# Kernel optimization log

Measured on AMD Instinct MI355X. Metric: run time of the kernel, lower is better.

Reference implementation:

```python
import jax, jax.numpy as jnp
import numpy as np

D_MODEL, N_HEADS, D_FF = 1024, 16, 4096
D_HEAD = D_MODEL // N_HEADS
B, S = 2, 2048
EPS = 1e-5


def setup_inputs() -> dict:
    key = jax.random.key(0)
    ks = jax.random.split(key, 12)
    sd = 1.0 / np.sqrt(D_MODEL)
    return {
        "x": jax.random.normal(ks[0], (B, S, D_MODEL), jnp.float32),
        "relative_bias": jax.random.normal(ks[1], (1, N_HEADS, S, S), jnp.float32),
        # attention projections, stored as (in, out) so y = x @ W
        "wq": jax.random.normal(ks[2], (D_MODEL, D_MODEL), jnp.float32) * sd,
        "wk": jax.random.normal(ks[3], (D_MODEL, D_MODEL), jnp.float32) * sd,
        "wv": jax.random.normal(ks[4], (D_MODEL, D_MODEL), jnp.float32) * sd,
        "wo": jax.random.normal(ks[5], (D_MODEL, D_MODEL), jnp.float32) * sd,
        "wo_b": jnp.zeros((D_MODEL,), jnp.float32),
        # FFN
        "w1": jax.random.normal(ks[6], (D_MODEL, D_FF), jnp.float32) * sd,
        "b1": jnp.zeros((D_FF,), jnp.float32),
        "w2": jax.random.normal(ks[7], (D_FF, D_MODEL), jnp.float32) * (1.0 / np.sqrt(D_FF)),
        "b2": jnp.zeros((D_MODEL,), jnp.float32),
        # LayerNorms
        "ln1_g": jnp.ones((D_MODEL,), jnp.float32),
        "ln1_b": jnp.zeros((D_MODEL,), jnp.float32),
        "ln2_g": jnp.ones((D_MODEL,), jnp.float32),
        "ln2_b": jnp.zeros((D_MODEL,), jnp.float32),
    }


def _layernorm(x, g, b):
    mu = jnp.mean(x, axis=-1, keepdims=True)
    var = jnp.mean(jnp.square(x - mu), axis=-1, keepdims=True)
    return (x - mu) * jax.lax.rsqrt(var + EPS) * g + b


def _attn(x, relative_bias, wq, wk, wv, wo, wo_b):
    b, s, d = x.shape
    # (B,S,D) -> (B,H,S,Dh)
    def split_heads(t):
        return t.reshape(b, s, N_HEADS, D_HEAD).transpose(0, 2, 1, 3)
    q = split_heads(x @ wq)
    k = split_heads(x @ wk)
    v = split_heads(x @ wv)
    scores = jnp.einsum("bhqd,bhkd->bhqk", q, k) / np.sqrt(D_HEAD) + relative_bias
    attn = jax.nn.softmax(scores, axis=-1)
    ctx = jnp.einsum("bhqk,bhkd->bhqd", attn, v)
    ctx = ctx.transpose(0, 2, 1, 3).reshape(b, s, d)
    return ctx @ wo + wo_b


def _ffn(x, w1, b1, w2, b2):
    return jax.nn.gelu(x @ w1 + b1, approximate=False) @ w2 + b2


def reference(x, relative_bias, wq, wk, wv, wo, wo_b, w1, b1, w2, b2,
              ln1_g, ln1_b, ln2_g, ln2_b):
    x = x + _attn(_layernorm(x, ln1_g, ln1_b), relative_bias, wq, wk, wv, wo, wo_b)
    x = x + _ffn(_layernorm(x, ln2_g, ln2_b), w1, b1, w2, b2)
    return x
```

## Files before the change

kernel.cpp:

```cpp
#include <hip/hip_runtime.h>
#include <hip/hip_bf16.h>
#include <stdint.h>

typedef unsigned short u16;
typedef __bf16 bf16x8 __attribute__((ext_vector_type(8)));
typedef u16   u16x8  __attribute__((ext_vector_type(8)));
typedef u16   u16x4  __attribute__((ext_vector_type(4)));
typedef u16   u16x2  __attribute__((ext_vector_type(2)));
typedef float f32x4  __attribute__((ext_vector_type(4)));

__device__ __forceinline__ u16 f2bf(float f) {
  union { float f; uint32_t u; } v; v.f = f;
  uint32_t r = v.u + 0x7fffu + ((v.u >> 16) & 1u);
  return (u16)(r >> 16);
}

typedef __attribute__((address_space(1))) void gvoid_t;
typedef __attribute__((address_space(3))) void lvoid_t;
__device__ __forceinline__ void gload_lds16(const void* g, void* l) {
  __builtin_amdgcn_global_load_lds((gvoid_t*)g, (lvoid_t*)l, 16, 0, 0);
}

__device__ __forceinline__ void barrier_lgkm() {
  asm volatile("s_waitcnt lgkmcnt(0)\ns_barrier" ::: "memory");
}
__device__ __forceinline__ void bar_only() {
  asm volatile("s_barrier" ::: "memory");
}
template<int N> __device__ __forceinline__ void wait_vm() {
  asm volatile("s_waitcnt vmcnt(%0)" :: "n"(N) : "memory");
}

template<int CTRL>
__device__ __forceinline__ float dpp_f(float x) {
  int i = __builtin_bit_cast(int, x);
  i = __builtin_amdgcn_update_dpp(i, i, CTRL, 0xF, 0xF, true);
  return __builtin_bit_cast(float, i);
}
__device__ __forceinline__ float rowmax16(float x) {
  x = fmaxf(x, dpp_f<0x128>(x));
  x = fmaxf(x, dpp_f<0x124>(x));
  x = fmaxf(x, dpp_f<0x122>(x));
  x = fmaxf(x, dpp_f<0x121>(x));
  return x;
}
__device__ __forceinline__ float rowsum16(float x) {
  x += dpp_f<0x128>(x);
  x += dpp_f<0x124>(x);
  x += dpp_f<0x122>(x);
  x += dpp_f<0x121>(x);
  return x;
}

__global__ __launch_bounds__(256)
void ln_kernel(const float* __restrict__ x, const float* __restrict__ g,
               const float* __restrict__ b, u16* __restrict__ out) {
  const int row = blockIdx.x;
  const int tid = threadIdx.x;
  const float* xr = x + (size_t)row * 1024;
  f32x4 v = *(const f32x4*)&xr[tid * 4];
  float s = v[0] + v[1] + v[2] + v[3];
  float q = v[0]*v[0] + v[1]*v[1] + v[2]*v[2] + v[3]*v[3];
  #pragma unroll
  for (int o = 32; o > 0; o >>= 1) { s += __shfl_xor(s, o); q += __shfl_xor(q, o); }
  __shared__ float ss[4], qq[4];
  if ((tid & 63) == 0) { ss[tid >> 6] = s; qq[tid >> 6] = q; }
  __syncthreads();
  s = ss[0] + ss[1] + ss[2] + ss[3];
  q = qq[0] + qq[1] + qq[2] + qq[3];
  float mu = s * (1.0f / 1024.0f);
  float var = q * (1.0f / 1024.0f) - mu * mu;
  float rstd = rsqrtf(var + 1e-5f);
  u16x4 o4;
  #pragma unroll
  for (int i = 0; i < 4; ++i)
    o4[i] = f2bf((v[i] - mu) * rstd * g[tid * 4 + i] + b[tid * 4 + i]);
  *(u16x4*)&out[(size_t)row * 1024 + tid * 4] = o4;
}

__global__ __launch_bounds__(256)
void transpose_cast(const float* __restrict__ W, u16* __restrict__ Wt, int K, int N) {
  __shared__ float t[32][33];
  const int n0 = blockIdx.x * 32, k0 = blockIdx.y * 32;
  const int tx = threadIdx.x & 31, ty = threadIdx.x >> 5;
  #pragma unroll
  for (int i = 0; i < 4; ++i)
    t[ty + 8*i][tx] = W[(size_t)(k0 + ty + 8*i) * N + n0 + tx];
  __syncthreads();
  #pragma unroll
  for (int i = 0; i < 4; ++i)
    Wt[(size_t)(n0 + ty + 8*i) * K + k0 + tx] = f2bf(t[tx][ty + 8*i]);
}

template<int EPI>
__global__ __launch_bounds__(256, 2)
void gemm_bt(const u16* __restrict__ A, const u16* __restrict__ Bt,
             void* __restrict__ out, const float* __restrict__ bias,
             const float* __restrict__ resid, int M, int N, int K) {
  __shared__ u16 As[2][128 * 32];
  __shared__ u16 Bs[2][128 * 32];
  const int tid = threadIdx.x;
  const int w = tid >> 6, l = tid & 63;
  const int bm = blockIdx.x * 128, bn = blockIdx.y * 128;
  const int wr = (w >> 1) * 64, wc = (w & 1) * 64;
  const int l15 = l & 15, lhi = l >> 4;
  f32x4 acc[4][4] = {};

  const int r4 = tid >> 2;
  const int c8 = (tid & 3) * 8;
  const u16* ga0 = A  + (size_t)(bm + r4) * K + c8;
  const u16* ga1 = ga0 + (size_t)64 * K;
  const u16* gb0 = Bt + (size_t)(bn + r4) * K + c8;
  const u16* gb1 = gb0 + (size_t)64 * K;

  const int arow = (wr + l15) * 32 + lhi * 8;
  const int brow = (wc + l15) * 32 + lhi * 8;

  auto stage = [&](int k0, int buf) {
    gload_lds16(ga0 + k0, &As[buf][(w * 16) * 32]);
    gload_lds16(ga1 + k0, &As[buf][(64 + w * 16) * 32]);
    gload_lds16(gb0 + k0, &Bs[buf][(w * 16) * 32]);
    gload_lds16(gb1 + k0, &Bs[buf][(64 + w * 16) * 32]);
  };

  const int nsteps = K >> 5;
  stage(0, 0);
  for (int s = 0; s < nsteps; ++s) {
    const int cur = s & 1;
    if (s + 1 < nsteps) { stage((s + 1) << 5, cur ^ 1); wait_vm<4>(); }
    else                { wait_vm<0>(); }
    bar_only();
    bf16x8 a[4], b[4];
    #pragma unroll
    for (int m = 0; m < 4; ++m) a[m] = *(const bf16x8*)&As[cur][arow + m * 16 * 32];
    #pragma unroll
    for (int n = 0; n < 4; ++n) b[n] = *(const bf16x8*)&Bs[cur][brow + n * 16 * 32];
    #pragma unroll
    for (int m = 0; m < 4; ++m)
      #pragma unroll
      for (int n = 0; n < 4; ++n)
        acc[m][n] = __builtin_amdgcn_mfma_f32_16x16x32_bf16(a[m], b[n], acc[m][n], 0, 0, 0);
    bar_only();
  }

  #pragma unroll
  for (int m = 0; m < 4; ++m) {
    #pragma unroll
    for (int n = 0; n < 4; ++n) {
      #pragma unroll
      for (int r = 0; r < 4; ++r) {
        const int grow = bm + wr + m * 16 + lhi * 4 + r;
        const int gcol = bn + wc + n * 16 + l15;
        float vv = acc[m][n][r];
        if constexpr (EPI >= 1) vv += bias[gcol];
        if constexpr (EPI == 1) vv = 0.5f * vv * (1.0f + erff(vv * 0.70710678118f));
        if constexpr (EPI == 2) {
          vv += resid[(size_t)grow * N + gcol];
          ((float*)out)[(size_t)grow * N + gcol] = vv;
        } else {
          ((u16*)out)[(size_t)grow * N + gcol] = f2bf(vv);
        }
      }
    }
  }
}

template<int EPI>
__global__ __launch_bounds__(256, 2)
void gemm_bt64(const u16* __restrict__ A, const u16* __restrict__ Bt,
               void* __restrict__ out, const float* __restrict__ bias,
               const float* __restrict__ resid, int M, int N, int K) {
  __shared__ u16 As[2][64 * 32];
  __shared__ u16 Bs[2][128 * 32];
  const int tid = threadIdx.x;
  const int w = tid >> 6, l = tid & 63;
  const int bm = blockIdx.x * 64, bn = blockIdx.y * 128;
  const int wr = (w & 1) * 32, wc = (w >> 1) * 64;
  const int l15 = l & 15, lhi = l >> 4;
  f32x4 acc[2][4] = {};

  const int r4 = tid >> 2;
  const int c8 = (tid & 3) * 8;
  const u16* ga0 = A  + (size_t)(bm + r4) * K + c8;
  const u16* gb0 = Bt + (size_t)(bn + r4) * K + c8;
  const u16* gb1 = gb0 + (size_t)64 * K;

  const int arow = (wr + l15) * 32 + lhi * 8;
  const int brow = (wc + l15) * 32 + lhi * 8;

  auto stage = [&](int k0, int buf) {
    gload_lds16(ga0 + k0, &As[buf][(w * 16) * 32]);
    gload_lds16(gb0 + k0, &Bs[buf][(w * 16) * 32]);
    gload_lds16(gb1 + k0, &Bs[buf][(64 + w * 16) * 32]);
  };

  const int nsteps = K >> 5;
  stage(0, 0);
  for (int s = 0; s < nsteps; ++s) {
    const int cur = s & 1;
    if (s + 1 < nsteps) { stage((s + 1) << 5, cur ^ 1); wait_vm<3>(); }
    else                { wait_vm<0>(); }
    bar_only();
    bf16x8 a[2], b[4];
    #pragma unroll
    for (int m = 0; m < 2; ++m) a[m] = *(const bf16x8*)&As[cur][arow + m * 16 * 32];
    #pragma unroll
    for (int n = 0; n < 4; ++n) b[n] = *(const bf16x8*)&Bs[cur][brow + n * 16 * 32];
    #pragma unroll
    for (int m = 0; m < 2; ++m)
      #pragma unroll
      for (int n = 0; n < 4; ++n)
        acc[m][n] = __builtin_amdgcn_mfma_f32_16x16x32_bf16(a[m], b[n], acc[m][n], 0, 0, 0);
    bar_only();
  }

  #pragma unroll
  for (int m = 0; m < 2; ++m) {
    #pragma unroll
    for (int n = 0; n < 4; ++n) {
      #pragma unroll
      for (int r = 0; r < 4; ++r) {
        const int grow = bm + wr + m * 16 + lhi * 4 + r;
        const int gcol = bn + wc + n * 16 + l15;
        float vv = acc[m][n][r];
        if constexpr (EPI >= 1) vv += bias[gcol];
        if constexpr (EPI == 1) vv = 0.5f * vv * (1.0f + erff(vv * 0.70710678118f));
        if constexpr (EPI == 2) {
          vv += resid[(size_t)grow * N + gcol];
          ((float*)out)[(size_t)grow * N + gcol] = vv;
        } else {
          ((u16*)out)[(size_t)grow * N + gcol] = f2bf(vv);
        }
      }
    }
  }
}

#define SWZ(row) ((((row) & 7) ^ (((row) >> 3) & 7)) << 3)

__global__ __launch_bounds__(256)
void attn_kernel(const u16* __restrict__ qkv, const float* __restrict__ bias,
                 u16* __restrict__ ctx) {
  const int qt = blockIdx.x;
  const int bh = blockIdx.y;
  const int b = bh >> 4, h = bh & 15;
  const int tid = threadIdx.x, w = tid >> 6, l = tid & 63;
  const int l15 = l & 15, lhi = l >> 4;
  const size_t ld = 3072;
  const float L2E = 1.44269504f;

  __shared__ u16 Kl[2][4096];
  __shared__ u16 Vt[2][4096];
  __shared__ u16 Pl[4][1024];

  const u16* qp = qkv;
  const u16* kp = qkv + 1024;
  const u16* vp = qkv + 2048;

  const int key2 = (tid >> 3) * 2, dg8 = (tid & 7) * 8;
  const u16* kbase = kp + ((size_t)b * 2048 + key2) * ld + h * 64 + dg8;
  const u16* vbase = vp + ((size_t)b * 2048 + key2) * ld + h * 64 + dg8;

  bf16x8 qf0, qf1;
  {
    const u16* qrow = qp + ((size_t)b * 2048 + qt * 64 + w * 16 + l15) * ld + h * 64 + lhi * 8;
    qf0 = *(const bf16x8*)qrow;
    qf1 = *(const bf16x8*)(qrow + 32);
  }

  const float* bg0 = bias + ((size_t)h * 2048 + qt * 64 + w * 16 + lhi * 4) * 2048 + l15;
  const float* bp0 = bg0;
  const float* bp1 = bg0 + 2048;
  const float* bp2 = bg0 + 4096;
  const float* bp3 = bg0 + 6144;

  float m_run[4], s_run[4];
  f32x4 octx[4] = {};
  #pragma unroll
  for (int r = 0; r < 4; ++r) { m_run[r] = -1e30f; s_run[r] = 0.f; }

  u16x8 kpf[2], vpf[2];
  float bfA[16], bfB[16];

  auto load_kv = [&](int kv) {
    kpf[0] = *(const u16x8*)(kbase + (size_t)kv * ld);
    kpf[1] = *(const u16x8*)(kbase + (size_t)(kv + 1) * ld);
    vpf[0] = *(const u16x8*)(vbase + (size_t)kv * ld);
    vpf[1] = *(const u16x8*)(vbase + (size_t)(kv + 1) * ld);
  };
  auto load_bias = [&](float (&bf)[16]) {
    bf[0]  = bp0[0];  bf[1]  = bp0[16]; bf[2]  = bp0[32]; bf[3]  = bp0[48];
    bf[4]  = bp1[0];  bf[5]  = bp1[16]; bf[6]  = bp1[32]; bf[7]  = bp1[48];
    bf[8]  = bp2[0];  bf[9]  = bp2[16]; bf[10] = bp2[32]; bf[11] = bp2[48];
    bf[12] = bp3[0];  bf[13] = bp3[16]; bf[14] = bp3[32]; bf[15] = bp3[48];
    bp0 += 64; bp1 += 64; bp2 += 64; bp3 += 64;
  };
  auto store_kv = [&](u16* Kd, u16* Vd) {
    *(u16x8*)&Kd[(key2)     * 64 + (dg8 ^ SWZ(key2))]     = kpf[0];
    *(u16x8*)&Kd[(key2 + 1) * 64 + (dg8 ^ SWZ(key2 + 1))] = kpf[1];
    #pragma unroll
    for (int i = 0; i < 8; ++i) {
      const int d = dg8 + i;
      u16x2 vq = { vpf[0][i], vpf[1][i] };
      *(u16x2*)&Vd[d * 64 + (key2 ^ SWZ(d))] = vq;
    }
  };

  load_kv(0);
  load_bias(bfA);
  load_bias(bfB);
  store_kv(Kl[0], Vt[0]);
  load_kv(64);
  barrier_lgkm();

  auto iter = [&](int it, int cur, float (&bc)[16]) {
    if (it < 31) store_kv(Kl[cur ^ 1], Vt[cur ^ 1]);
    if (it < 30) load_kv((it + 2) * 64);

    f32x4 sa[4] = {};
    #pragma unroll
    for (int nf = 0; nf < 4; ++nf) {
      const int row = nf * 16 + l15;
      const int s = SWZ(row);
      bf16x8 kf0 = *(const bf16x8*)&Kl[cur][row * 64 + ((lhi * 8) ^ s)];
      bf16x8 kf1 = *(const bf16x8*)&Kl[cur][row * 64 + ((32 + lhi * 8) ^ s)];
      sa[nf] = __builtin_amdgcn_mfma_f32_16x16x32_bf16(qf0, kf0, sa[nf], 0, 0, 0);
      sa[nf] = __builtin_amdgcn_mfma_f32_16x16x32_bf16(qf1, kf1, sa[nf], 0, 0, 0);
    }

    float p[4][4];
    #pragma unroll
    for (int r = 0; r < 4; ++r)
      #pragma unroll
      for (int nf = 0; nf < 4; ++nf)
        p[r][nf] = fmaf(sa[nf][r], 0.125f, bc[r * 4 + nf]);
    if (it < 30) load_bias(bc);

    #pragma unroll
    for (int r = 0; r < 4; ++r) {
      float mx = fmaxf(fmaxf(p[r][0], p[r][1]), fmaxf(p[r][2], p[r][3]));
      mx = rowmax16(mx);
      if (mx > m_run[r] + 5.545177f) {
        const float fs = exp2f((m_run[r] - mx) * L2E);
        s_run[r] *= fs;
        #pragma unroll
        for (int nf = 0; nf < 4; ++nf) octx[nf][r] *= fs;
        m_run[r] = mx;
      }
      const float nml = -m_run[r] * L2E;
      float e0 = exp2f(fmaf(p[r][0], L2E, nml));
      float e1 = exp2f(fmaf(p[r][1], L2E, nml));
      float e2 = exp2f(fmaf(p[r][2], L2E, nml));
      float e3 = exp2f(fmaf(p[r][3], L2E, nml));
      p[r][0] = e0; p[r][1] = e1; p[r][2] = e2; p[r][3] = e3;
      s_run[r] += rowsum16((e0 + e1) + (e2 + e3));
    }

    #pragma unroll
    for (int r = 0; r < 4; ++r) {
      const int row = lhi * 4 + r;
      const int s = SWZ(row);
      #pragma unroll
      for (int nf = 0; nf < 4; ++nf)
        Pl[w][row * 64 + ((nf * 16 + l15) ^ s)] =
            __builtin_bit_cast(u16, (__bf16)p[r][nf]);
    }

    #pragma unroll
    for (int ks = 0; ks < 2; ++ks) {
      bf16x8 pa = *(const bf16x8*)&Pl[w][l15 * 64 + ((ks * 32 + lhi * 8) ^ SWZ(l15))];
      #pragma unroll
      for (int nf = 0; nf < 4; ++nf) {
        const int row = nf * 16 + l15;
        bf16x8 bv = *(const bf16x8*)&Vt[cur][row * 64 + ((ks * 32 + lhi * 8) ^ SWZ(row))];
        octx[nf] = __builtin_amdgcn_mfma_f32_16x16x32_bf16(pa, bv, octx[nf], 0, 0, 0);
      }
    }

    barrier_lgkm();
  };

  for (int i2 = 0; i2 < 16; ++i2) {
    iter(2 * i2,     0, bfA);
    iter(2 * i2 + 1, 1, bfB);
  }

  float inv[4];
  #pragma unroll
  for (int r = 0; r < 4; ++r) inv[r] = 1.0f / s_run[r];
  #pragma unroll
  for (int nf = 0; nf < 4; ++nf)
    #pragma unroll
    for (int r = 0; r < 4; ++r) {
      const int grow = b * 2048 + qt * 64 + w * 16 + lhi * 4 + r;
      const int gcol = h * 64 + nf * 16 + l15;
      ctx[(size_t)grow * 1024 + gcol] = f2bf(octx[nf][r] * inv[r]);
    }
}

extern "C" void kernel_launch(void* const* d_in, const int* in_sizes, int n_in,
                              void* d_out, int out_size, void* d_ws, size_t ws_size,
                              hipStream_t stream) {
  const float* x    = (const float*)d_in[0];
  const float* rb   = (const float*)d_in[1];
  const float* wq   = (const float*)d_in[2];
  const float* wk   = (const float*)d_in[3];
  const float* wv   = (const float*)d_in[4];
  const float* wo   = (const float*)d_in[5];
  const float* wo_b = (const float*)d_in[6];
  const float* w1   = (const float*)d_in[7];
  const float* b1   = (const float*)d_in[8];
  const float* w2   = (const float*)d_in[9];
  const float* b2   = (const float*)d_in[10];
  const float* ln1g = (const float*)d_in[11];
  const float* ln1b = (const float*)d_in[12];
  const float* ln2g = (const float*)d_in[13];
  const float* ln2b = (const float*)d_in[14];

  char* ws = (char*)d_ws;
  u16*   xn    = (u16*)(ws + 0);
  u16*   qkvb  = (u16*)(ws + (8u << 20));
  u16*   hbuf  = (u16*)(ws + (8u << 20));
  u16*   ctxb  = (u16*)(ws + (32u << 20));
  float* x1    = (float*)(ws + (40u << 20));
  u16*   wqkvt = (u16*)(ws + (56u << 20));
  u16*   wot   = (u16*)(ws + (62u << 20));
  u16*   w1t   = (u16*)(ws + (64u << 20));
  u16*   w2t   = (u16*)(ws + (72u << 20));

  transpose_cast<<<dim3(32, 32),  256, 0, stream>>>(wq, wqkvt,               1024, 1024);
  transpose_cast<<<dim3(32, 32),  256, 0, stream>>>(wk, wqkvt + 1024 * 1024, 1024, 1024);
  transpose_cast<<<dim3(32, 32),  256, 0, stream>>>(wv, wqkvt + 2048 * 1024, 1024, 1024);
  transpose_cast<<<dim3(32, 32),  256, 0, stream>>>(wo, wot,                 1024, 1024);
  transpose_cast<<<dim3(128, 32), 256, 0, stream>>>(w1, w1t,                 1024, 4096);
  transpose_cast<<<dim3(32, 128), 256, 0, stream>>>(w2, w2t,                 4096, 1024);

  ln_kernel<<<4096, 256, 0, stream>>>(x, ln1g, ln1b, xn);
  gemm_bt<0><<<dim3(32, 24), 256, 0, stream>>>(xn, wqkvt, qkvb, nullptr, nullptr, 4096, 3072, 1024);
  attn_kernel<<<dim3(32, 32), 256, 0, stream>>>(qkvb, rb, ctxb);
  gemm_bt64<2><<<dim3(64, 8), 256, 0, stream>>>(ctxb, wot, x1, wo_b, x, 4096, 1024, 1024);
  ln_kernel<<<4096, 256, 0, stream>>>(x1, ln2g, ln2b, xn);
  gemm_bt<1><<<dim3(32, 32), 256, 0, stream>>>(xn, w1t, hbuf, b1, nullptr, 4096, 4096, 1024);
  gemm_bt64<2><<<dim3(64, 8), 256, 0, stream>>>(hbuf, w2t, (float*)d_out, b2, x1, 4096, 1024, 4096);

  (void)in_sizes; (void)n_in; (void)out_size; (void)ws_size;
}
```

Measured before the change: 390.6 us.

## Transpose QK^T MFMA so each lane owns one query row in softmax

Swaps the MFMA operand order for the score computation so each lane holds four consecutive keys of a single query row instead of four rows. Bias can then be loaded as f32x4 vectors rather than scalar gathers, and softmax max/sum need one in-register reduction plus two cross-lane shuffles instead of per-row DPP reductions. Rescale factors and the final normaliser are broadcast back to the P·V accumulator layout with shuffles, and P is written to LDS as 4-wide packed stores. The cost is extra shuffles on the rescale path, which now runs whenever any lane in the wave needs it.

```diff
diff --git a/kernel.cpp b/kernel.cpp
--- a/kernel.cpp
+++ b/kernel.cpp
@@ -29,27 +29,6 @@
 }
 template<int N> __device__ __forceinline__ void wait_vm() {
   asm volatile("s_waitcnt vmcnt(%0)" :: "n"(N) : "memory");
-}
-
-template<int CTRL>
-__device__ __forceinline__ float dpp_f(float x) {
-  int i = __builtin_bit_cast(int, x);
-  i = __builtin_amdgcn_update_dpp(i, i, CTRL, 0xF, 0xF, true);
-  return __builtin_bit_cast(float, i);
-}
-__device__ __forceinline__ float rowmax16(float x) {
-  x = fmaxf(x, dpp_f<0x128>(x));
-  x = fmaxf(x, dpp_f<0x124>(x));
-  x = fmaxf(x, dpp_f<0x122>(x));
-  x = fmaxf(x, dpp_f<0x121>(x));
-  return x;
-}
-__device__ __forceinline__ float rowsum16(float x) {
-  x += dpp_f<0x128>(x);
-  x += dpp_f<0x124>(x);
-  x += dpp_f<0x122>(x);
-  x += dpp_f<0x121>(x);
-  return x;
 }
 
 __global__ __launch_bounds__(256)
@@ -268,19 +247,13 @@
     qf1 = *(const bf16x8*)(qrow + 32);
   }
 
-  const float* bg0 = bias + ((size_t)h * 2048 + qt * 64 + w * 16 + lhi * 4) * 2048 + l15;
-  const float* bp0 = bg0;
-  const float* bp1 = bg0 + 2048;
-  const float* bp2 = bg0 + 4096;
-  const float* bp3 = bg0 + 6144;
-
-  float m_run[4], s_run[4];
+  const float* bp = bias + ((size_t)h * 2048 + qt * 64 + w * 16 + l15) * 2048 + lhi * 4;
+
+  float m_run = -1e30f, s_run = 0.f;
   f32x4 octx[4] = {};
-  #pragma unroll
-  for (int r = 0; r < 4; ++r) { m_run[r] = -1e30f; s_run[r] = 0.f; }
 
   u16x8 kpf[2], vpf[2];
-  float bfA[16], bfB[16];
+  f32x4 bfA[4], bfB[4];
 
   auto load_kv = [&](int kv) {
     kpf[0] = *(const u16x8*)(kbase + (size_t)kv * ld);
@@ -288,12 +261,10 @@
     vpf[0] = *(const u16x8*)(vbase + (size_t)kv * ld);
     vpf[1] = *(const u16x8*)(vbase + (size_t)(kv + 1) * ld);
   };
-  auto load_bias = [&](float (&bf)[16]) {
-    bf[0]  = bp0[0];  bf[1]  = bp0[16]; bf[2]  = bp0[32]; bf[3]  = bp0[48];
-    bf[4]  = bp1[0];  bf[5]  = bp1[16]; bf[6]  = bp1[32]; bf[7]  = bp1[48];
-    bf[8]  = bp2[0];  bf[9]  = bp2[16]; bf[10] = bp2[32]; bf[11] = bp2[48];
-    bf[12] = bp3[0];  bf[13] = bp3[16]; bf[14] = bp3[32]; bf[15] = bp3[48];
-    bp0 += 64; bp1 += 64; bp2 += 64; bp3 += 64;
+  auto load_bias = [&](f32x4 (&bv)[4]) {
+    #pragma unroll
+    for (int nf = 0; nf < 4; ++nf) bv[nf] = *(const f32x4*)(bp + nf * 16);
+    bp += 64;
   };
   auto store_kv = [&](u16* Kd, u16* Vd) {
     *(u16x8*)&Kd[(key2)     * 64 + (dg8 ^ SWZ(key2))]     = kpf[0];
@@ -313,7 +284,7 @@
   load_kv(64);
   barrier_lgkm();
 
-  auto iter = [&](int it, int cur, float (&bc)[16]) {
+  auto iter = [&](int it, int cur, f32x4 (&bc)[4]) {
     if (it < 31) store_kv(Kl[cur ^ 1], Vt[cur ^ 1]);
     if (it < 30) load_kv((it + 2) * 64);
 
@@ -324,46 +295,69 @@
       const int s = SWZ(row);
       bf16x8 kf0 = *(const bf16x8*)&Kl[cur][row * 64 + ((lhi * 8) ^ s)];
       bf16x8 kf1 = *(const bf16x8*)&Kl[cur][row * 64 + ((32 + lhi * 8) ^ s)];
-      sa[nf] = __builtin_amdgcn_mfma_f32_16x16x32_bf16(qf0, kf0, sa[nf], 0, 0, 0);
-      sa[nf] = __builtin_amdgcn_mfma_f32_16x16x32_bf16(qf1, kf1, sa[nf], 0, 0, 0);
-    }
-
-    float p[4][4];
-    #pragma unroll
-    for (int r = 0; r < 4; ++r)
-      #pragma unroll
-      for (int nf = 0; nf < 4; ++nf)
-        p[r][nf] = fmaf(sa[nf][r], 0.125f, bc[r * 4 + nf]);
+      sa[nf] = __builtin_amdgcn_mfma_f32_16x16x32_bf16(kf0, qf0, sa[nf], 0, 0, 0);
+      sa[nf] = __builtin_amdgcn_mfma_f32_16x16x32_bf16(kf1, qf1, sa[nf], 0, 0, 0);
+    }
+
+    f32x4 p[4];
+    #pragma unroll
+    for (int nf = 0; nf < 4; ++nf)
+      #pragma unroll
+      for (int j = 0; j < 4; ++j)
+        p[nf][j] = fmaf(sa[nf][j], 0.125f, bc[nf][j]);
     if (it < 30) load_bias(bc);
 
-    #pragma unroll
-    for (int r = 0; r < 4; ++r) {
-      float mx = fmaxf(fmaxf(p[r][0], p[r][1]), fmaxf(p[r][2], p[r][3]));
-      mx = rowmax16(mx);
-      if (mx > m_run[r] + 5.545177f) {
-        const float fs = exp2f((m_run[r] - mx) * L2E);
-        s_run[r] *= fs;
-        #pragma unroll
-        for (int nf = 0; nf < 4; ++nf) octx[nf][r] *= fs;
-        m_run[r] = mx;
+    f32x4 m4;
+    #pragma unroll
+    for (int j = 0; j < 4; ++j)
+      m4[j] = fmaxf(fmaxf(p[0][j], p[1][j]), fmaxf(p[2][j], p[3][j]));
+    float mx = fmaxf(fmaxf(m4[0], m4[1]), fmaxf(m4[2], m4[3]));
+    mx = fmaxf(mx, __shfl_xor(mx, 16));
+    mx = fmaxf(mx, __shfl_xor(mx, 32));
+
+    if (__any(mx > m_run + 5.545177f)) {
+      const bool c = mx > m_run + 5.545177f;
+      const float mnew = c ? mx : m_run;
+      const float fs = exp2f((m_run - mnew) * L2E);
+      s_run *= fs; m_run = mnew;
+      const float f0 = __shfl(fs, lhi * 4 + 0);
+      const float f1 = __shfl(fs, lhi * 4 + 1);
+      const float f2 = __shfl(fs, lhi * 4 + 2);
+      const float f3 = __shfl(fs, lhi * 4 + 3);
+      #pragma unroll
+      for (int nf = 0; nf < 4; ++nf) {
+        octx[nf][0] *= f0; octx[nf][1] *= f1;
+        octx[nf][2] *= f2; octx[nf][3] *= f3;
       }
-      const float nml = -m_run[r] * L2E;
-      float e0 = exp2f(fmaf(p[r][0], L2E, nml));
-      float e1 = exp2f(fmaf(p[r][1], L2E, nml));
-      float e2 = exp2f(fmaf(p[r][2], L2E, nml));
-      float e3 = exp2f(fmaf(p[r][3], L2E, nml));
-      p[r][0] = e0; p[r][1] = e1; p[r][2] = e2; p[r][3] = e3;
-      s_run[r] += rowsum16((e0 + e1) + (e2 + e3));
-    }
-
-    #pragma unroll
-    for (int r = 0; r < 4; ++r) {
-      const int row = lhi * 4 + r;
-      const int s = SWZ(row);
-      #pragma unroll
-      for (int nf = 0; nf < 4; ++nf)
-        Pl[w][row * 64 + ((nf * 16 + l15) ^ s)] =
-            __builtin_bit_cast(u16, (__bf16)p[r][nf]);
+    }
+
+    const float nml = -m_run * L2E;
+    f32x4 e[4];
+    #pragma unroll
+    for (int nf = 0; nf < 4; ++nf)
+      #pragma unroll
+      for (int j = 0; j < 4; ++j)
+        e[nf][j] = exp2f(fmaf(p[nf][j], L2E, nml));
+    f32x4 s4;
+    #pragma unroll
+    for (int j = 0; j < 4; ++j)
+      s4[j] = (e[0][j] + e[1][j]) + (e[2][j] + e[3][j]);
+    float ps = (s4[0] + s4[1]) + (s4[2] + s4[3]);
+    ps += __shfl_xor(ps, 16);
+    ps += __shfl_xor(ps, 32);
+    s_run += ps;
+
+    {
+      const int sw = SWZ(l15);
+      const int base = l15 * 64;
+      #pragma unroll
+      for (int nf = 0; nf < 4; ++nf) {
+        u16x4 pk = { __builtin_bit_cast(u16, (__bf16)e[nf][0]),
+                     __builtin_bit_cast(u16, (__bf16)e[nf][1]),
+                     __builtin_bit_cast(u16, (__bf16)e[nf][2]),
+                     __builtin_bit_cast(u16, (__bf16)e[nf][3]) };
+        *(u16x4*)&Pl[w][base + ((nf * 16 + lhi * 4) ^ sw)] = pk;
+      }
     }
 
     #pragma unroll
@@ -385,16 +379,19 @@
     iter(2 * i2 + 1, 1, bfB);
   }
 
-  float inv[4];
-  #pragma unroll
-  for (int r = 0; r < 4; ++r) inv[r] = 1.0f / s_run[r];
+  const float inv = 1.0f / s_run;
+  float invr[4];
+  invr[0] = __shfl(inv, lhi * 4 + 0);
+  invr[1] = __shfl(inv, lhi * 4 + 1);
+  invr[2] = __shfl(inv, lhi * 4 + 2);
+  invr[3] = __shfl(inv, lhi * 4 + 3);
   #pragma unroll
   for (int nf = 0; nf < 4; ++nf)
     #pragma unroll
     for (int r = 0; r < 4; ++r) {
       const int grow = b * 2048 + qt * 64 + w * 16 + lhi * 4 + r;
       const int gcol = h * 64 + nf * 16 + l15;
-      ctx[(size_t)grow * 1024 + gcol] = f2bf(octx[nf][r] * inv[r]);
+      ctx[(size_t)grow * 1024 + gcol] = f2bf(octx[nf][r] * invr[r]);
     }
 }
 
```

Result: faster. 382.8 us (-2.0%).
